# Kernel optimization log

Measured on AMD Instinct MI355X. Metric: run time of the kernel, lower is better.

The kernel has to match this reference:

```python
import jax, jax.numpy as jnp
import numpy as np

M, K, N = 8192, 4096, 4096  # tokens, in_features, out_features


def setup_inputs() -> dict:
    key = jax.random.key(0)
    k1, k2, k3, k4 = jax.random.split(key, 4)
    inp = jax.random.normal(k1, (M, K), dtype=jnp.float32)
    # int8-range weights stored as int32 host-side; [out_features, in_features] like torch Linear
    weight = jax.random.randint(k2, (N, K), -128, 128, dtype=jnp.int32)
    weight_scale = jax.random.uniform(k3, (N,), dtype=jnp.float32, minval=1e-3, maxval=2e-2)
    bias = jax.random.normal(k4, (N,), dtype=jnp.float32)
    return {"input": inp, "weight": weight, "weight_scale": weight_scale, "bias": bias}


def reference(input, weight, weight_scale, bias):
    # --- init-time transforms (W8A8IntLinear.__init__) ---
    wq = weight.T.astype(jnp.int8)                                   # [K, N]
    azp_adj = jnp.sum(wq.astype(jnp.int32), axis=0, keepdims=True)    # [1, N] int32 column sums

    # --- dynamic asymmetric per-token int8 quantization (scaled_int8_quant) ---
    x_max = jnp.max(input, axis=-1, keepdims=True)                    # [M, 1]
    x_min = jnp.min(input, axis=-1, keepdims=True)                    # [M, 1]
    scale = (x_max - x_min) / 255.0                                   # per-token scale
    azp = jnp.round(-128.0 - x_min / scale).astype(jnp.int32)         # per-token zero point
    q = jnp.clip(jnp.round(input / scale).astype(jnp.int32) + azp, -128, 127).astype(jnp.int8)

    # --- int8 GEMM with int32 accumulation (cutlass_scaled_mm_azp) ---
    acc = jnp.matmul(q, wq, preferred_element_type=jnp.int32)         # [M, N] int32
    corrected = (acc - azp * azp_adj).astype(jnp.float32)             # zero-point correction
    return scale * weight_scale[None, :] * corrected + bias[None, :]
```

## Files before the change

kernel.cpp:

```cpp
#include <hip/hip_runtime.h>
#include <cstdint>
#include <cstddef>


#define M_DIM 8192
#define K_DIM 4096
#define N_DIM 4096

typedef int v4i __attribute__((ext_vector_type(4)));

__global__ __launch_bounds__(256) void quant_kernel(
    const float* __restrict__ x, signed char* __restrict__ q,
    float* __restrict__ scale_out, int* __restrict__ azp_out)
{
    const int m = blockIdx.x;
    const int t = threadIdx.x;
    const float4* row4 = (const float4*)(x + (size_t)m * K_DIM);

    float4 v[4];
    float mx = -3.4e38f, mn = 3.4e38f;
#pragma unroll
    for (int i = 0; i < 4; ++i) {
        v[i] = row4[i * 256 + t];
        mx = fmaxf(mx, fmaxf(fmaxf(v[i].x, v[i].y), fmaxf(v[i].z, v[i].w)));
        mn = fminf(mn, fminf(fminf(v[i].x, v[i].y), fminf(v[i].z, v[i].w)));
    }
#pragma unroll
    for (int off = 32; off; off >>= 1) {
        mx = fmaxf(mx, __shfl_down(mx, off));
        mn = fminf(mn, __shfl_down(mn, off));
    }
    __shared__ float smx[4], smn[4];
    if ((t & 63) == 0) { smx[t >> 6] = mx; smn[t >> 6] = mn; }
    __syncthreads();
    mx = fmaxf(fmaxf(smx[0], smx[1]), fmaxf(smx[2], smx[3]));
    mn = fminf(fminf(smn[0], smn[1]), fminf(smn[2], smn[3]));

    const float scale = (mx - mn) / 255.0f;
    const int azp = (int)rintf(-128.0f - mn / scale);
    if (t == 0) { scale_out[m] = scale; azp_out[m] = azp; }

    int* qrow = (int*)(q + (size_t)m * K_DIM);
    const float* vf = (const float*)v;
#pragma unroll
    for (int i = 0; i < 4; ++i) {
        int b[4];
#pragma unroll
        for (int j = 0; j < 4; ++j) {
            int qv = (int)rintf(vf[4 * i + j] / scale) + azp;
            qv = qv < -128 ? -128 : (qv > 127 ? 127 : qv);
            b[j] = qv;
        }
        qrow[i * 256 + t] =
            (b[0] & 255) | ((b[1] & 255) << 8) | ((b[2] & 255) << 16) | ((b[3] & 255) << 24);
    }
}

__global__ __launch_bounds__(256) void wprep_kernel(
    const int* __restrict__ w, signed char* __restrict__ w8, int* __restrict__ azp_adj)
{
    const int n = blockIdx.x;
    const int t = threadIdx.x;
    const int4* row = (const int4*)(w + (size_t)n * K_DIM);
    int* w8row = (int*)(w8 + (size_t)n * K_DIM);
    int sum = 0;
#pragma unroll
    for (int i = 0; i < 4; ++i) {
        int4 a = row[i * 256 + t];
        sum += a.x + a.y + a.z + a.w;
        w8row[i * 256 + t] =
            (a.x & 255) | ((a.y & 255) << 8) | ((a.z & 255) << 16) | ((a.w & 255) << 24);
    }
#pragma unroll
    for (int off = 32; off; off >>= 1) sum += __shfl_down(sum, off);
    __shared__ int ssum[4];
    if ((t & 63) == 0) ssum[t >> 6] = sum;
    __syncthreads();
    if (t == 0) azp_adj[n] = ssum[0] + ssum[1] + ssum[2] + ssum[3];
}

__device__ __forceinline__ void async_copy16(const signed char* g, signed char* l) {
    __builtin_amdgcn_global_load_lds(
        (const __attribute__((address_space(1))) void*)g,
        (__attribute__((address_space(3))) void*)l, 16, 0, 0);
}

__global__ __launch_bounds__(256) void gemm_kernel(
    const signed char* __restrict__ A,
    const signed char* __restrict__ B,
    const float* __restrict__ scale, const int* __restrict__ azp,
    const int* __restrict__ azp_adj, const float* __restrict__ wscale,
    const float* __restrict__ bias, float* __restrict__ out)
{
    __shared__ signed char sA[128 * 64];
    __shared__ signed char sB[128 * 64];

    const int t = threadIdx.x;
    const int wave = t >> 6;
    const int lane = t & 63;
    const int quad = lane >> 4;
    const int r16 = lane & 15;

    const int bm = blockIdx.y * 128;
    const int bn = blockIdx.x * 128;
    const int wm = (wave >> 1) * 64;
    const int wn = (wave & 1) * 64;

    v4i acc[4][4];
#pragma unroll
    for (int i = 0; i < 4; ++i)
#pragma unroll
        for (int j = 0; j < 4; ++j) acc[i][j] = (v4i){0, 0, 0, 0};

    const int srow = t >> 2;
    const int scol = ((t & 3) ^ ((t >> 3) & 3)) * 16;
    const signed char* ag0 = A + (size_t)(bm + srow) * K_DIM + scol;
    const signed char* ag1 = A + (size_t)(bm + 64 + srow) * K_DIM + scol;
    const signed char* bg0 = B + (size_t)(bn + srow) * K_DIM + scol;
    const signed char* bg1 = B + (size_t)(bn + 64 + srow) * K_DIM + scol;

    const v4i* sA4 = (const v4i*)sA;
    const v4i* sB4 = (const v4i*)sB;

    for (int k0 = 0; k0 < K_DIM; k0 += 64) {
        async_copy16(ag0 + k0, sA + t * 16);
        async_copy16(ag1 + k0, sA + 4096 + t * 16);
        async_copy16(bg0 + k0, sB + t * 16);
        async_copy16(bg1 + k0, sB + 4096 + t * 16);
        __syncthreads();

        v4i af[4], bf[4];
#pragma unroll
        for (int i = 0; i < 4; ++i) {
            const int ra = wm + i * 16 + r16;
            const int rb = wn + i * 16 + r16;
            af[i] = sA4[ra * 4 + (quad ^ ((ra >> 1) & 3))];
            bf[i] = sB4[rb * 4 + (quad ^ ((rb >> 1) & 3))];
        }
#pragma unroll
        for (int i = 0; i < 4; ++i)
#pragma unroll
            for (int j = 0; j < 4; ++j)
                acc[i][j] = __builtin_amdgcn_mfma_i32_16x16x64_i8(af[i], bf[j], acc[i][j], 0, 0, 0);
        __syncthreads();
    }

#pragma unroll
    for (int i = 0; i < 4; ++i) {
        const int mbase = bm + wm + i * 16 + quad * 4;
        float sm[4]; int am[4];
#pragma unroll
        for (int r = 0; r < 4; ++r) { sm[r] = scale[mbase + r]; am[r] = azp[mbase + r]; }
#pragma unroll
        for (int j = 0; j < 4; ++j) {
            const int n = bn + wn + j * 16 + r16;
            const float wsn = wscale[n];
            const int adjn = azp_adj[n];
            const float bn_ = bias[n];
#pragma unroll
            for (int r = 0; r < 4; ++r) {
                const int c = acc[i][j][r] - am[r] * adjn;
                out[(size_t)(mbase + r) * N_DIM + n] = sm[r] * wsn * (float)c + bn_;
            }
        }
    }
}

extern "C" void kernel_launch(void* const* d_in, const int* in_sizes, int n_in,
                              void* d_out, int out_size, void* d_ws, size_t ws_size,
                              hipStream_t stream) {
    const float* x      = (const float*)d_in[0];
    const int*   w      = (const int*)d_in[1];
    const float* wscale = (const float*)d_in[2];
    const float* bias   = (const float*)d_in[3];
    float* out = (float*)d_out;

    char* ws = (char*)d_ws;
    signed char* q8  = (signed char*)ws;
    signed char* w8  = (signed char*)(ws + 33554432);
    float* scl       = (float*)(ws + 50331648);
    int*   azp       = (int*)(ws + 50331648 + 32768);
    int*   adj       = (int*)(ws + 50331648 + 65536);

    quant_kernel<<<M_DIM, 256, 0, stream>>>(x, q8, scl, azp);
    wprep_kernel<<<N_DIM, 256, 0, stream>>>(w, w8, adj);
    dim3 grid(N_DIM / 128, M_DIM / 128);
    gemm_kernel<<<grid, 256, 0, stream>>>(q8, w8, scl, azp, adj, wscale, bias, out);
}
```

Baseline: 433.3 us.

## Use 256x256 GEMM tiles with 4-stage async LDS pipeline and merged prep kernel

Result: faster. 410.1 us (-5.4%).

```diff
diff --git a/kernel.cpp b/kernel.cpp
--- a/kernel.cpp
+++ b/kernel.cpp
@@ -6,77 +6,77 @@
 #define M_DIM 8192
 #define K_DIM 4096
 #define N_DIM 4096
+#define NT (K_DIM / 64)
 
 typedef int v4i __attribute__((ext_vector_type(4)));
 
-__global__ __launch_bounds__(256) void quant_kernel(
+__global__ __launch_bounds__(256) void prep_kernel(
     const float* __restrict__ x, signed char* __restrict__ q,
-    float* __restrict__ scale_out, int* __restrict__ azp_out)
+    float* __restrict__ scale_out, int* __restrict__ azp_out,
+    const int* __restrict__ w, signed char* __restrict__ w8,
+    int* __restrict__ azp_adj)
 {
-    const int m = blockIdx.x;
     const int t = threadIdx.x;
-    const float4* row4 = (const float4*)(x + (size_t)m * K_DIM);
-
-    float4 v[4];
-    float mx = -3.4e38f, mn = 3.4e38f;
-#pragma unroll
-    for (int i = 0; i < 4; ++i) {
-        v[i] = row4[i * 256 + t];
-        mx = fmaxf(mx, fmaxf(fmaxf(v[i].x, v[i].y), fmaxf(v[i].z, v[i].w)));
-        mn = fminf(mn, fminf(fminf(v[i].x, v[i].y), fminf(v[i].z, v[i].w)));
+    if (blockIdx.x < M_DIM) {
+        const int m = blockIdx.x;
+        const float4* row4 = (const float4*)(x + (size_t)m * K_DIM);
+
+        float4 v[4];
+        float mx = -3.4e38f, mn = 3.4e38f;
+#pragma unroll
+        for (int i = 0; i < 4; ++i) {
+            v[i] = row4[i * 256 + t];
+            mx = fmaxf(mx, fmaxf(fmaxf(v[i].x, v[i].y), fmaxf(v[i].z, v[i].w)));
+            mn = fminf(mn, fminf(fminf(v[i].x, v[i].y), fminf(v[i].z, v[i].w)));
+        }
+#pragma unroll
+        for (int off = 32; off; off >>= 1) {
+            mx = fmaxf(mx, __shfl_down(mx, off));
+            mn = fminf(mn, __shfl_down(mn, off));
+        }
+        __shared__ float smx[4], smn[4];
+        if ((t & 63) == 0) { smx[t >> 6] = mx; smn[t >> 6] = mn; }
+        __syncthreads();
+        mx = fmaxf(fmaxf(smx[0], smx[1]), fmaxf(smx[2], smx[3]));
+        mn = fminf(fminf(smn[0], smn[1]), fminf(smn[2], smn[3]));
+
+        const float scale = (mx - mn) / 255.0f;
+        const int azp = (int)rintf(-128.0f - mn / scale);
+        if (t == 0) { scale_out[m] = scale; azp_out[m] = azp; }
+
+        int* qrow = (int*)(q + (size_t)m * K_DIM);
+        const float* vf = (const float*)v;
+#pragma unroll
+        for (int i = 0; i < 4; ++i) {
+            int b[4];
+#pragma unroll
+            for (int j = 0; j < 4; ++j) {
+                int qv = (int)rintf(vf[4 * i + j] / scale) + azp;
+                qv = qv < -128 ? -128 : (qv > 127 ? 127 : qv);
+                b[j] = qv;
+            }
+            qrow[i * 256 + t] =
+                (b[0] & 255) | ((b[1] & 255) << 8) | ((b[2] & 255) << 16) | ((b[3] & 255) << 24);
+        }
+    } else {
+        const int n = blockIdx.x - M_DIM;
+        const int4* row = (const int4*)(w + (size_t)n * K_DIM);
+        int* w8row = (int*)(w8 + (size_t)n * K_DIM);
+        int sum = 0;
+#pragma unroll
+        for (int i = 0; i < 4; ++i) {
+            int4 a = row[i * 256 + t];
+            sum += a.x + a.y + a.z + a.w;
+            w8row[i * 256 + t] =
+                (a.x & 255) | ((a.y & 255) << 8) | ((a.z & 255) << 16) | ((a.w & 255) << 24);
+        }
+#pragma unroll
+        for (int off = 32; off; off >>= 1) sum += __shfl_down(sum, off);
+        __shared__ int ssum[4];
+        if ((t & 63) == 0) ssum[t >> 6] = sum;
+        __syncthreads();
+        if (t == 0) azp_adj[n] = ssum[0] + ssum[1] + ssum[2] + ssum[3];
     }
-#pragma unroll
-    for (int off = 32; off; off >>= 1) {
-        mx = fmaxf(mx, __shfl_down(mx, off));
-        mn = fminf(mn, __shfl_down(mn, off));
-    }
-    __shared__ float smx[4], smn[4];
-    if ((t & 63) == 0) { smx[t >> 6] = mx; smn[t >> 6] = mn; }
-    __syncthreads();
-    mx = fmaxf(fmaxf(smx[0], smx[1]), fmaxf(smx[2], smx[3]));
-    mn = fminf(fminf(smn[0], smn[1]), fminf(smn[2], smn[3]));
-
-    const float scale = (mx - mn) / 255.0f;
-    const int azp = (int)rintf(-128.0f - mn / scale);
-    if (t == 0) { scale_out[m] = scale; azp_out[m] = azp; }
-
-    int* qrow = (int*)(q + (size_t)m * K_DIM);
-    const float* vf = (const float*)v;
-#pragma unroll
-    for (int i = 0; i < 4; ++i) {
-        int b[4];
-#pragma unroll
-        for (int j = 0; j < 4; ++j) {
-            int qv = (int)rintf(vf[4 * i + j] / scale) + azp;
-            qv = qv < -128 ? -128 : (qv > 127 ? 127 : qv);
-            b[j] = qv;
-        }
-        qrow[i * 256 + t] =
-            (b[0] & 255) | ((b[1] & 255) << 8) | ((b[2] & 255) << 16) | ((b[3] & 255) << 24);
-    }
-}
-
-__global__ __launch_bounds__(256) void wprep_kernel(
-    const int* __restrict__ w, signed char* __restrict__ w8, int* __restrict__ azp_adj)
-{
-    const int n = blockIdx.x;
-    const int t = threadIdx.x;
-    const int4* row = (const int4*)(w + (size_t)n * K_DIM);
-    int* w8row = (int*)(w8 + (size_t)n * K_DIM);
-    int sum = 0;
-#pragma unroll
-    for (int i = 0; i < 4; ++i) {
-        int4 a = row[i * 256 + t];
-        sum += a.x + a.y + a.z + a.w;
-        w8row[i * 256 + t] =
-            (a.x & 255) | ((a.y & 255) << 8) | ((a.z & 255) << 16) | ((a.w & 255) << 24);
-    }
-#pragma unroll
-    for (int off = 32; off; off >>= 1) sum += __shfl_down(sum, off);
-    __shared__ int ssum[4];
-    if ((t & 63) == 0) ssum[t >> 6] = sum;
-    __syncthreads();
-    if (t == 0) azp_adj[n] = ssum[0] + ssum[1] + ssum[2] + ssum[3];
 }
 
 __device__ __forceinline__ void async_copy16(const signed char* g, signed char* l) {
@@ -85,68 +85,112 @@
         (__attribute__((address_space(3))) void*)l, 16, 0, 0);
 }
 
-__global__ __launch_bounds__(256) void gemm_kernel(
+__global__ __launch_bounds__(512, 2) void gemm_kernel(
     const signed char* __restrict__ A,
     const signed char* __restrict__ B,
     const float* __restrict__ scale, const int* __restrict__ azp,
     const int* __restrict__ azp_adj, const float* __restrict__ wscale,
     const float* __restrict__ bias, float* __restrict__ out)
 {
-    __shared__ signed char sA[128 * 64];
-    __shared__ signed char sB[128 * 64];
+    __shared__ signed char sA[4][16384];
+    __shared__ signed char sB[4][16384];
 
     const int t = threadIdx.x;
+    const int lane = t & 63;
     const int wave = t >> 6;
-    const int lane = t & 63;
     const int quad = lane >> 4;
     const int r16 = lane & 15;
 
-    const int bm = blockIdx.y * 128;
-    const int bn = blockIdx.x * 128;
-    const int wm = (wave >> 1) * 64;
-    const int wn = (wave & 1) * 64;
-
-    v4i acc[4][4];
-#pragma unroll
-    for (int i = 0; i < 4; ++i)
+    int bid = blockIdx.y * gridDim.x + blockIdx.x;
+    bid = (bid & 7) * 64 + (bid >> 3);
+    const int bn = (bid & 15) << 8;
+    const int bm = (bid >> 4) << 8;
+
+    const int wm = (wave >> 2) << 7;
+    const int wn = (wave & 3) << 6;
+
+    v4i acc[8][4];
+#pragma unroll
+    for (int i = 0; i < 8; ++i)
 #pragma unroll
         for (int j = 0; j < 4; ++j) acc[i][j] = (v4i){0, 0, 0, 0};
 
     const int srow = t >> 2;
-    const int scol = ((t & 3) ^ ((t >> 3) & 3)) * 16;
+    const int scol = ((t & 3) ^ ((t >> 3) & 3)) << 4;
     const signed char* ag0 = A + (size_t)(bm + srow) * K_DIM + scol;
-    const signed char* ag1 = A + (size_t)(bm + 64 + srow) * K_DIM + scol;
+    const signed char* ag1 = A + (size_t)(bm + 128 + srow) * K_DIM + scol;
     const signed char* bg0 = B + (size_t)(bn + srow) * K_DIM + scol;
-    const signed char* bg1 = B + (size_t)(bn + 64 + srow) * K_DIM + scol;
-
-    const v4i* sA4 = (const v4i*)sA;
-    const v4i* sB4 = (const v4i*)sB;
-
-    for (int k0 = 0; k0 < K_DIM; k0 += 64) {
-        async_copy16(ag0 + k0, sA + t * 16);
-        async_copy16(ag1 + k0, sA + 4096 + t * 16);
-        async_copy16(bg0 + k0, sB + t * 16);
-        async_copy16(bg1 + k0, sB + 4096 + t * 16);
-        __syncthreads();
+    const signed char* bg1 = B + (size_t)(bn + 128 + srow) * K_DIM + scol;
+
+#define STAGE_A(kt) do { const int _b = (kt) & 3; const int _ko = (kt) << 6; \
+    async_copy16(ag0 + _ko, &sA[_b][t * 16]); \
+    async_copy16(ag1 + _ko, &sA[_b][8192 + t * 16]); } while (0)
+#define STAGE_B(kt) do { const int _b = (kt) & 3; const int _ko = (kt) << 6; \
+    async_copy16(bg0 + _ko, &sB[_b][t * 16]); \
+    async_copy16(bg1 + _ko, &sB[_b][8192 + t * 16]); } while (0)
+
+    STAGE_A(0); STAGE_B(0);
+    STAGE_A(1); STAGE_B(1);
+    STAGE_A(2); STAGE_B(2);
+    asm volatile("s_waitcnt vmcnt(8)" ::: "memory");
+    __builtin_amdgcn_s_barrier();
+
+    const int swz = quad ^ ((r16 >> 1) & 3);
+
+    for (int kt = 0; kt < NT; ++kt) {
+        const int b = kt & 3;
+        const v4i* a4 = (const v4i*)&sA[b][0];
+        const v4i* b4 = (const v4i*)&sB[b][0];
 
         v4i af[4], bf[4];
 #pragma unroll
         for (int i = 0; i < 4; ++i) {
-            const int ra = wm + i * 16 + r16;
-            const int rb = wn + i * 16 + r16;
-            af[i] = sA4[ra * 4 + (quad ^ ((ra >> 1) & 3))];
-            bf[i] = sB4[rb * 4 + (quad ^ ((rb >> 1) & 3))];
-        }
+            af[i] = a4[(wm + i * 16 + r16) * 4 + swz];
+            bf[i] = b4[(wn + i * 16 + r16) * 4 + swz];
+        }
+        if (kt < NT - 3) STAGE_A(kt + 3);
+        asm volatile("" ::: "memory");
+        __builtin_amdgcn_s_barrier();
+        asm volatile("s_waitcnt lgkmcnt(0)" ::: "memory");
+        __builtin_amdgcn_s_setprio(1);
 #pragma unroll
         for (int i = 0; i < 4; ++i)
 #pragma unroll
             for (int j = 0; j < 4; ++j)
                 acc[i][j] = __builtin_amdgcn_mfma_i32_16x16x64_i8(af[i], bf[j], acc[i][j], 0, 0, 0);
-        __syncthreads();
+        __builtin_amdgcn_s_setprio(0);
+        asm volatile("" ::: "memory");
+        __builtin_amdgcn_s_barrier();
+
+        v4i ah[4];
+#pragma unroll
+        for (int i = 0; i < 4; ++i)
+            ah[i] = a4[(wm + 64 + i * 16 + r16) * 4 + swz];
+        if (kt < NT - 3) STAGE_B(kt + 3);
+        asm volatile("" ::: "memory");
+        __builtin_amdgcn_s_barrier();
+        asm volatile("s_waitcnt lgkmcnt(0)" ::: "memory");
+        __builtin_amdgcn_s_setprio(1);
+#pragma unroll
+        for (int i = 0; i < 4; ++i)
+#pragma unroll
+            for (int j = 0; j < 4; ++j)
+                acc[4 + i][j] = __builtin_amdgcn_mfma_i32_16x16x64_i8(ah[i], bf[j], acc[4 + i][j], 0, 0, 0);
+        __builtin_amdgcn_s_setprio(0);
+
+        if (kt < NT - 1) {
+            if (kt < NT - 3)        asm volatile("s_waitcnt vmcnt(8)" ::: "memory");
+            else if (kt == NT - 3)  asm volatile("s_waitcnt vmcnt(4)" ::: "memory");
+            else                    asm volatile("s_waitcnt vmcnt(0)" ::: "memory");
+            __builtin_amdgcn_s_barrier();
+        }
     }
 
-#pragma unroll
-    for (int i = 0; i < 4; ++i) {
+#undef STAGE_A
+#undef STAGE_B
+
+#pragma unroll
+    for (int i = 0; i < 8; ++i) {
         const int mbase = bm + wm + i * 16 + quad * 4;
         float sm[4]; int am[4];
 #pragma unroll
@@ -182,8 +226,7 @@
     int*   azp       = (int*)(ws + 50331648 + 32768);
     int*   adj       = (int*)(ws + 50331648 + 65536);
 
-    quant_kernel<<<M_DIM, 256, 0, stream>>>(x, q8, scl, azp);
-    wprep_kernel<<<N_DIM, 256, 0, stream>>>(w, w8, adj);
-    dim3 grid(N_DIM / 128, M_DIM / 128);
-    gemm_kernel<<<grid, 256, 0, stream>>>(q8, w8, scl, azp, adj, wscale, bias, out);
-}
+    prep_kernel<<<M_DIM + N_DIM, 256, 0, stream>>>(x, q8, scl, azp, w, w8, adj);
+    dim3 grid(N_DIM / 256, M_DIM / 256);
+    gemm_kernel<<<grid, 512, 0, stream>>>(q8, w8, scl, azp, adj, wscale, bias, out);
+}
```
